# Performance work log

Hardware: AMD Instinct MI355X
Metric: run time of the kernel (lower is better)

The kernel has to match this reference:

```python
import jax, jax.numpy as jnp
import numpy as np

NH = 16      # n_head
HS = 64      # head_size
BD = 16      # bond_dim
HORIZON = 64
C = NH * HS  # n_embd = 1024


def setup_inputs() -> dict:
    key = jax.random.key(0)
    ks = jax.random.split(key, 16)
    B, T = 2, 1024
    s = lambda fan_in: 1.0 / np.sqrt(fan_in)
    inp = {
        'x': jax.random.normal(ks[0], (B, T, C), dtype=jnp.float32),
        # all linear weights stored (in, out) for x @ W
        'W_disp': jax.random.normal(ks[1], (C, NH * BD), dtype=jnp.float32) * s(C),
        'b_disp': jnp.zeros((NH * BD,), dtype=jnp.float32),
        'W_val': jax.random.normal(ks[2], (C, C), dtype=jnp.float32) * s(C),
        'b_val': jnp.zeros((C,), dtype=jnp.float32),
        'rel_pos_emb': jax.random.normal(ks[3], (HORIZON, BD), dtype=jnp.float32) * 0.02,
        'W_fused': jax.random.normal(ks[4], (BD, 2 * BD), dtype=jnp.float32) * s(BD),
        'b_fused': jnp.zeros((2 * BD,), dtype=jnp.float32),
        'W_pos': jax.random.normal(ks[5], (BD, BD), dtype=jnp.float32) * s(BD),
        'W_bond': jax.random.normal(ks[6], (BD, 1), dtype=jnp.float32) * s(BD),
        'b_bond': jnp.zeros((1,), dtype=jnp.float32),
        'W_dmg': jax.random.normal(ks[7], (BD, 1), dtype=jnp.float32) * s(BD),
        'b_dmg': jnp.full((1,), -3.0, dtype=jnp.float32),  # nn.init.constant_(-3.0)
        'W_cproj': jax.random.normal(ks[8], (C, C), dtype=jnp.float32) * s(C),
        'b_cproj': jnp.zeros((C,), dtype=jnp.float32),
    }
    return inp


def reference(x, W_disp, b_disp, W_val, b_val, rel_pos_emb, W_fused, b_fused,
              W_pos, W_bond, b_bond, W_dmg, b_dmg, W_cproj, b_cproj):
    B, T, Cm = x.shape
    delta = min(HORIZON, T)
    # projections -> (B, nh, T, d)
    disp = (x @ W_disp + b_disp).reshape(B, T, NH, BD).transpose(0, 2, 1, 3)
    val = (x @ W_val + b_val).reshape(B, T, NH, HS).transpose(0, 2, 1, 3)
    idx = jnp.arange(T)[:, None] + jnp.arange(delta)[None, :]  # (T, delta)
    disp_p = jnp.pad(disp, ((0, 0), (0, 0), (delta - 1, 0), (0, 0)))
    win = disp_p[:, :, idx]                       # (B, nh, T, delta, bd)
    strain = win - disp[:, :, :, None, :]         # (B, nh, T, delta, bd)
    pos_feat = rel_pos_emb @ W_pos                # (delta, bd)
    fused = strain @ W_fused + b_fused            # (B, nh, T, delta, 2*bd)
    bf, df = fused[..., :BD], fused[..., BD:]
    gelu = lambda z: jax.nn.gelu(z, approximate=False)
    bond_logits = (gelu(bf + pos_feat) @ W_bond + b_bond)[..., 0]   # (B,nh,T,delta)
    damage = jax.nn.sigmoid((gelu(df) @ W_dmg + b_dmg)[..., 0])
    bond_logits = bond_logits - damage * 10.0
    # causal validity mask: position t - delta + 1 + j must be >= 0
    cmask = (jnp.arange(T)[:, None] - delta + 1 + jnp.arange(delta)[None, :]) >= 0
    bond_logits = jnp.where(cmask[None, None], bond_logits, -jnp.inf)
    weights = jax.nn.softmax(bond_logits, axis=-1)
    val_p = jnp.pad(val, ((0, 0), (0, 0), (delta - 1, 0), (0, 0)))
    vwin = val_p[:, :, idx]                       # (B, nh, T, delta, hs)
    out = jnp.einsum('bhtd,bhtdk->bhtk', weights, vwin)  # (B, nh, T, hs)
    out = out.transpose(0, 2, 1, 3).reshape(B, T, Cm)
    return out @ W_cproj + b_cproj
```

## Files before the change

### kernel.cpp

```cpp
#include <hip/hip_runtime.h>
#include <math.h>


typedef __attribute__((ext_vector_type(4))) float f32x4;
typedef __attribute__((ext_vector_type(8))) __bf16 bf16x8;

__device__ __forceinline__ ushort f2bf(float f) {
    union { float f; unsigned u; } v; v.f = f;
    const unsigned r = v.u + 0x7fffu + ((v.u >> 16) & 1u);
    return (ushort)(r >> 16);
}

__device__ __forceinline__ float gelu_fast(float z) {
    const float a = -1.5957691216057308f * z * fmaf(0.044715f, z * z, 1.0f);
    return z * __builtin_amdgcn_rcpf(1.0f + __expf(a));
}

__global__ __launch_bounds__(256) void gemm_bf16_kernel(
    const ushort* __restrict__ A, const ushort* __restrict__ Bt,
    const float* __restrict__ bias, float* __restrict__ C,
    int M, int N, int K)
{
    __shared__ ushort As[64 * 64];
    __shared__ ushort Bs[64 * 64];
    const int tid  = threadIdx.x;
    const int wave = tid >> 6;
    const int lane = tid & 63;
    const int rowbase = blockIdx.y * 64;
    const int colbase = blockIdx.x * 64;
    const int wr = wave >> 1;
    const int wc = wave & 1;

    f32x4 acc[2][2] = {};

    for (int k0 = 0; k0 < K; k0 += 64) {
        #pragma unroll
        for (int i = 0; i < 2; ++i) {
            const int p   = i * 256 + tid;
            const int row = p >> 3;
            const int kc  = (p & 7) ^ (row & 7);
            const ushort* srcA = A + (size_t)(rowbase + row) * K + k0 + kc * 8;
            __builtin_amdgcn_global_load_lds(
                (const __attribute__((address_space(1))) void*)srcA,
                (__attribute__((address_space(3))) void*)(As + (size_t)p * 8),
                16, 0, 0);
            const ushort* srcB = Bt + (size_t)(colbase + row) * K + k0 + kc * 8;
            __builtin_amdgcn_global_load_lds(
                (const __attribute__((address_space(1))) void*)srcB,
                (__attribute__((address_space(3))) void*)(Bs + (size_t)p * 8),
                16, 0, 0);
        }
        __syncthreads();

        #pragma unroll
        for (int kk = 0; kk < 2; ++kk) {
            const int kb = kk * 32 + (lane >> 4) * 8;
            bf16x8 a[2], b[2];
            #pragma unroll
            for (int ni = 0; ni < 2; ++ni) {
                const int n = wc * 32 + ni * 16 + (lane & 15);
                const int off = (n * 128 + kb * 2) ^ ((n & 7) << 4);
                b[ni] = *(const bf16x8*)((const char*)Bs + off);
            }
            #pragma unroll
            for (int mi = 0; mi < 2; ++mi) {
                const int r = wr * 32 + mi * 16 + (lane & 15);
                const int off = (r * 128 + kb * 2) ^ ((r & 7) << 4);
                a[mi] = *(const bf16x8*)((const char*)As + off);
            }
            #pragma unroll
            for (int mi = 0; mi < 2; ++mi)
                #pragma unroll
                for (int ni = 0; ni < 2; ++ni)
                    acc[mi][ni] = __builtin_amdgcn_mfma_f32_16x16x32_bf16(
                        a[mi], b[ni], acc[mi][ni], 0, 0, 0);
        }
        __syncthreads();
    }

    #pragma unroll
    for (int mi = 0; mi < 2; ++mi)
        #pragma unroll
        for (int ni = 0; ni < 2; ++ni) {
            const int col = colbase + wc * 32 + ni * 16 + (lane & 15);
            const float bvc = bias[col];
            #pragma unroll
            for (int r = 0; r < 4; ++r) {
                const int row = rowbase + wr * 32 + mi * 16 + (lane >> 4) * 4 + r;
                C[(size_t)row * N + col] = acc[mi][ni][r] + bvc;
            }
        }
}

__global__ __launch_bounds__(256) void gemm_qv_kernel(
    const ushort* __restrict__ Acat,
    const ushort* __restrict__ xb,
    const float* __restrict__ b_val,
    float* __restrict__ dprojT,
    ushort* __restrict__ valT)
{
    __shared__ ushort As[128 * 64];
    __shared__ ushort Bs[64 * 64];
    const int tid  = threadIdx.x;
    const int wave = tid >> 6;
    const int lane = tid & 63;
    const int rowbase = blockIdx.y * 128;
    const int colbase = blockIdx.x * 64;
    const int wr = wave >> 1;
    const int wc = wave & 1;

    f32x4 acc[4][2] = {};

    for (int k0 = 0; k0 < 1024; k0 += 64) {
        #pragma unroll
        for (int i = 0; i < 4; ++i) {
            const int p   = i * 256 + tid;
            const int row = p >> 3;
            const int kc  = (p & 7) ^ (row & 7);
            const ushort* srcA = Acat + (size_t)(rowbase + row) * 1024 + k0 + kc * 8;
            __builtin_amdgcn_global_load_lds(
                (const __attribute__((address_space(1))) void*)srcA,
                (__attribute__((address_space(3))) void*)(As + (size_t)p * 8),
                16, 0, 0);
        }
        #pragma unroll
        for (int i = 0; i < 2; ++i) {
            const int p   = i * 256 + tid;
            const int row = p >> 3;
            const int kc  = (p & 7) ^ (row & 7);
            const ushort* srcB = xb + (size_t)(colbase + row) * 1024 + k0 + kc * 8;
            __builtin_amdgcn_global_load_lds(
                (const __attribute__((address_space(1))) void*)srcB,
                (__attribute__((address_space(3))) void*)(Bs + (size_t)p * 8),
                16, 0, 0);
        }
        __syncthreads();

        #pragma unroll
        for (int kk = 0; kk < 2; ++kk) {
            const int kb = kk * 32 + (lane >> 4) * 8;
            bf16x8 a[4], b[2];
            #pragma unroll
            for (int ni = 0; ni < 2; ++ni) {
                const int n = wc * 32 + ni * 16 + (lane & 15);
                const int off = (n * 128 + kb * 2) ^ ((n & 7) << 4);
                b[ni] = *(const bf16x8*)((const char*)Bs + off);
            }
            #pragma unroll
            for (int mi = 0; mi < 4; ++mi) {
                const int r = wr * 64 + mi * 16 + (lane & 15);
                const int off = (r * 128 + kb * 2) ^ ((r & 7) << 4);
                a[mi] = *(const bf16x8*)((const char*)As + off);
            }
            #pragma unroll
            for (int mi = 0; mi < 4; ++mi)
                #pragma unroll
                for (int ni = 0; ni < 2; ++ni)
                    acc[mi][ni] = __builtin_amdgcn_mfma_f32_16x16x32_bf16(
                        a[mi], b[ni], acc[mi][ni], 0, 0, 0);
        }
        __syncthreads();
    }

    if (rowbase < 512) {
        #pragma unroll
        for (int mi = 0; mi < 4; ++mi)
            #pragma unroll
            for (int ni = 0; ni < 2; ++ni) {
                const int col = colbase + wc * 32 + ni * 16 + (lane & 15);
                #pragma unroll
                for (int r = 0; r < 4; ++r) {
                    const int row = rowbase + wr * 64 + mi * 16 + (lane >> 4) * 4 + r;
                    dprojT[(size_t)row * 2048 + col] = acc[mi][ni][r];
                }
            }
    } else {
        #pragma unroll
        for (int mi = 0; mi < 4; ++mi)
            #pragma unroll
            for (int ni = 0; ni < 2; ++ni) {
                const int col = colbase + wc * 32 + ni * 16 + (lane & 15);
                #pragma unroll
                for (int r = 0; r < 4; ++r) {
                    const int row = rowbase - 512 + wr * 64 + mi * 16 + (lane >> 4) * 4 + r;
                    valT[(size_t)row * 2048 + col] = f2bf(acc[mi][ni][r] + b_val[row]);
                }
            }
    }
}

__global__ __launch_bounds__(256) void prep_kernel(
    const float* __restrict__ x,
    const float* __restrict__ W_disp,
    const float* __restrict__ W_val,
    const float* __restrict__ W_cproj,
    const float* __restrict__ W_fused,
    const float* __restrict__ rel,
    const float* __restrict__ Wpos,
    ushort* __restrict__ xb,
    ushort* __restrict__ Acat,
    ushort* __restrict__ WcT,
    float* __restrict__ posf)
{
    __shared__ float shmem[64 * 65];
    const int bid = blockIdx.x, tid = threadIdx.x;

    if (bid < 2048) {
        const int idx = bid * 256 + tid;
        const float4 v = reinterpret_cast<const float4*>(x)[idx];
        ushort4 o; o.x = f2bf(v.x); o.y = f2bf(v.y); o.z = f2bf(v.z); o.w = f2bf(v.w);
        reinterpret_cast<ushort4*>(xb)[idx] = o;
    } else if (bid < 2560) {
        const int isC = bid >= 2304;
        const int b2 = bid - (isC ? 2304 : 2048);
        const float* W = isC ? W_cproj : W_val;
        ushort* Wt = isC ? WcT : (Acat + 512 * 1024);
        const int n0 = (b2 & 15) * 64;
        const int k0 = (b2 >> 4) * 64;
        float (*tile)[65] = (float (*)[65])shmem;
        #pragma unroll
        for (int i = 0; i < 4; ++i) {
            const int idx = tid + i * 256;
            const int r = idx >> 4;
            const int c = (idx & 15) << 2;
            const float4 v = *reinterpret_cast<const float4*>(
                W + (size_t)(k0 + r) * 1024 + n0 + c);
            tile[r][c] = v.x; tile[r][c+1] = v.y; tile[r][c+2] = v.z; tile[r][c+3] = v.w;
        }
        __syncthreads();
        #pragma unroll
        for (int i = 0; i < 4; ++i) {
            const int idx = tid + i * 256;
            const int n = idx >> 4;
            const int c = (idx & 15) << 2;
            ushort4 o;
            o.x = f2bf(tile[c][n]);     o.y = f2bf(tile[c + 1][n]);
            o.z = f2bf(tile[c + 2][n]); o.w = f2bf(tile[c + 3][n]);
            *reinterpret_cast<ushort4*>(Wt + (size_t)(n0 + n) * 1024 + k0 + c) = o;
        }
    } else if (bid < 4608) {
        float* wfs = shmem;
        for (int i = tid; i < 512; i += 256) wfs[i] = W_fused[i];
        __syncthreads();
        const int idx = (bid - 2560) * 256 + tid;
        const int cc = idx >> 10;
        const int r  = idx & 1023;
        const int h = cc >> 5, e = cc & 31;
        const float* wd = W_disp + r * 256 + h * 16;
        float s = 0.f;
        #pragma unroll
        for (int d = 0; d < 16; ++d) s += wd[d] * wfs[d * 32 + e];
        Acat[idx] = f2bf(s);
    } else {
        for (int n = tid; n < 1024; n += 256) {
            const int j = n >> 4, e = n & 15;
            float s = 0.f;
            #pragma unroll
            for (int k = 0; k < 16; ++k) s += rel[j * 16 + k] * Wpos[k * 16 + e];
            posf[n] = s;
        }
    }
}

__global__ __launch_bounds__(256) void weights_kernel(
    const float* __restrict__ dprojT,
    const float* __restrict__ posf_g,
    const float* __restrict__ bfused,
    const float* __restrict__ Wbond,
    const float* __restrict__ bbond,
    const float* __restrict__ Wdmg,
    const float* __restrict__ bdmg,
    ushort* __restrict__ wout)
{
    __shared__ float dwin[32][68];
    __shared__ float sbd[16];
    __shared__ float wbd[16];
    __shared__ float wdm[16];
    const int tid  = threadIdx.x;
    const int wave = tid >> 6;
    const int lane = tid & 63;
    const int bh = blockIdx.x >> 8;
    const int t0 = (blockIdx.x & 255) * 4;
    const int h  = bh & 15;
    const int b  = bh >> 4;

    if (tid < 16) {
        sbd[tid] = bfused[16 + tid];
        wbd[tid] = Wbond[tid];
        wdm[tid] = Wdmg[tid];
    }
    const float* dbase = dprojT + (size_t)(h * 32) * 2048 + b * 1024;
    {
        const int r = tid & 63;
        int grow = t0 - 63 + r;
        grow = grow < 0 ? 0 : grow;
        #pragma unroll
        for (int i = 0; i < 8; ++i) {
            const int c = (tid >> 6) + i * 4;
            dwin[c][r] = dbase[(size_t)c * 2048 + grow];
        }
    }
    if (tid < 128) {
        const int c = tid >> 2;
        const int rs = tid & 3;
        if (rs < 3) {
            const int r = 64 + rs;
            int grow = t0 - 63 + r;
            dwin[c][r] = dbase[(size_t)c * 2048 + grow];
        }
    }
    float sbp[16];
    {
        const float4 p0 = *reinterpret_cast<const float4*>(posf_g + lane * 16);
        const float4 p1 = *reinterpret_cast<const float4*>(posf_g + lane * 16 + 4);
        const float4 p2 = *reinterpret_cast<const float4*>(posf_g + lane * 16 + 8);
        const float4 p3 = *reinterpret_cast<const float4*>(posf_g + lane * 16 + 12);
        sbp[0] = p0.x; sbp[1] = p0.y; sbp[2]  = p0.z; sbp[3]  = p0.w;
        sbp[4] = p1.x; sbp[5] = p1.y; sbp[6]  = p1.z; sbp[7]  = p1.w;
        sbp[8] = p2.x; sbp[9] = p2.y; sbp[10] = p2.z; sbp[11] = p2.w;
        sbp[12] = p3.x; sbp[13] = p3.y; sbp[14] = p3.z; sbp[15] = p3.w;
        #pragma unroll
        for (int e = 0; e < 16; ++e) sbp[e] += bfused[e];
    }
    __syncthreads();

    const int t = t0 + wave;
    const int tsrc = t + lane - 63;
    const int rw = wave + lane;
    const int rt = wave + 63;

    float bond = bbond[0];
    float dmg  = bdmg[0];
    #pragma unroll
    for (int e = 0; e < 16; ++e) {
        bond += gelu_fast(dwin[e][rw] - dwin[e][rt] + sbp[e]) * wbd[e];
        dmg  += gelu_fast(dwin[16 + e][rw] - dwin[16 + e][rt] + sbd[e]) * wdm[e];
    }
    const float damage = __builtin_amdgcn_rcpf(1.0f + __expf(-dmg));
    float logit = bond - 10.0f * damage;
    if (tsrc < 0) logit = -INFINITY;

    float m = logit;
    #pragma unroll
    for (int o = 32; o; o >>= 1) m = fmaxf(m, __shfl_xor(m, o));
    const float p = __expf(logit - m);
    float ssum = p;
    #pragma unroll
    for (int o = 32; o; o >>= 1) ssum += __shfl_xor(ssum, o);
    wout[(size_t)(bh * 1024 + t) * 64 + lane] = f2bf(p * __builtin_amdgcn_rcpf(ssum));
}

__global__ __launch_bounds__(256) void pv_kernel(
    const ushort* __restrict__ valT,
    const ushort* __restrict__ w,
    ushort* __restrict__ attnb)
{
    __shared__ ushort Ps[64 * 128];
    __shared__ ushort Vs[64 * 128];
    const int tid  = threadIdx.x;
    const int wave = tid >> 6;
    const int lane = tid & 63;
    const int bh = blockIdx.x >> 4;
    const int t0 = (blockIdx.x & 15) * 64;
    const int b  = bh >> 4;
    const int h  = bh & 15;

    #pragma unroll
    for (int i = 0; i < 4; ++i) {
        const int p = i * 256 + tid;
        const int c = p >> 4, q = p & 15;
        const int kc = q ^ (c & 7);
        int tt = t0 - 64 + kc * 8;
        tt = tt < 0 ? 0 : tt;
        const ushort* src = valT + (size_t)(h * 64 + c) * 2048 + b * 1024 + tt;
        __builtin_amdgcn_global_load_lds(
            (const __attribute__((address_space(1))) void*)src,
            (__attribute__((address_space(3))) void*)(Vs + (size_t)p * 8),
            16, 0, 0);
    }
    #pragma unroll
    for (int i = 0; i < 4; ++i)
        reinterpret_cast<uint4*>(Ps)[i * 256 + tid] = uint4{0, 0, 0, 0};
    __syncthreads();
    #pragma unroll
    for (int i = 0; i < 16; ++i) {
        const int n  = i * 256 + tid;
        const int ti = n >> 6, jj = n & 63;
        const ushort wv = w[((size_t)bh * 1024 + t0 + ti) * 64 + jj];
        const int off = (ti * 256 + (ti + jj + 1) * 2) ^ ((ti & 7) << 4);
        *(ushort*)((char*)Ps + off) = wv;
    }
    __syncthreads();

    const int wr = wave >> 1;
    const int wc = wave & 1;
    f32x4 acc[2][2] = {};
    #pragma unroll
    for (int kk = 0; kk < 4; ++kk) {
        const int kb = kk * 32 + (lane >> 4) * 8;
        bf16x8 a[2], bv[2];
        #pragma unroll
        for (int ni = 0; ni < 2; ++ni) {
            const int cc = wc * 32 + ni * 16 + (lane & 15);
            const int off = (cc * 256 + kb * 2) ^ ((cc & 7) << 4);
            bv[ni] = *(const bf16x8*)((const char*)Vs + off);
        }
        #pragma unroll
        for (int mi = 0; mi < 2; ++mi) {
            const int rr = wr * 32 + mi * 16 + (lane & 15);
            const int off = (rr * 256 + kb * 2) ^ ((rr & 7) << 4);
            a[mi] = *(const bf16x8*)((const char*)Ps + off);
        }
        #pragma unroll
        for (int mi = 0; mi < 2; ++mi)
            #pragma unroll
            for (int ni = 0; ni < 2; ++ni)
                acc[mi][ni] = __builtin_amdgcn_mfma_f32_16x16x32_bf16(
                    a[mi], bv[ni], acc[mi][ni], 0, 0, 0);
    }

    #pragma unroll
    for (int mi = 0; mi < 2; ++mi)
        #pragma unroll
        for (int ni = 0; ni < 2; ++ni) {
            const int c = wc * 32 + ni * 16 + (lane & 15);
            #pragma unroll
            for (int r = 0; r < 4; ++r) {
                const int trow = t0 + wr * 32 + mi * 16 + (lane >> 4) * 4 + r;
                attnb[(size_t)(b * 1024 + trow) * 1024 + h * 64 + c] =
                    f2bf(acc[mi][ni][r]);
            }
        }
}

extern "C" void kernel_launch(void* const* d_in, const int* in_sizes, int n_in,
                              void* d_out, int out_size, void* d_ws, size_t ws_size,
                              hipStream_t stream) {
    const float* x       = (const float*)d_in[0];
    const float* W_disp  = (const float*)d_in[1];
    const float* W_val   = (const float*)d_in[3];
    const float* b_val   = (const float*)d_in[4];
    const float* rel     = (const float*)d_in[5];
    const float* W_fused = (const float*)d_in[6];
    const float* b_fused = (const float*)d_in[7];
    const float* W_pos   = (const float*)d_in[8];
    const float* W_bond  = (const float*)d_in[9];
    const float* b_bond  = (const float*)d_in[10];
    const float* W_dmg   = (const float*)d_in[11];
    const float* b_dmg   = (const float*)d_in[12];
    const float* W_cproj = (const float*)d_in[13];
    const float* b_cproj = (const float*)d_in[14];
    float* out = (float*)d_out;

    ushort* Acat   = (ushort*)d_ws;
    ushort* xb     = Acat + 1536 * 1024;
    ushort* WcT    = xb + 2048 * 1024;
    float*  dprojT = (float*)(WcT + 1024 * 1024);
    ushort* valT   = (ushort*)(dprojT + 512 * 2048);
    ushort* wbuf   = valT + 1024 * 2048;
    ushort* attnb  = wbuf + 32768 * 64;
    float*  posf   = (float*)(attnb + 2048 * 1024);

    dim3 blk(256);
    prep_kernel<<<dim3(4609), blk, 0, stream>>>(
        x, W_disp, W_val, W_cproj, W_fused, rel, W_pos, xb, Acat, WcT, posf);
    gemm_qv_kernel<<<dim3(2048 / 64, 1536 / 128), blk, 0, stream>>>(
        Acat, xb, b_val, dprojT, valT);
    weights_kernel<<<dim3(8192), blk, 0, stream>>>(
        dprojT, posf, b_fused, W_bond, b_bond, W_dmg, b_dmg, wbuf);
    pv_kernel<<<dim3(512), blk, 0, stream>>>(valT, wbuf, attnb);
    gemm_bf16_kernel<<<dim3(1024 / 64, 2048 / 64), blk, 0, stream>>>(
        attnb, WcT, b_cproj, out, 2048, 1024, 1024);
}
```

Before: 76.89 us.

## Fuse bond-weight softmax into PV kernel, swizzle GEMM blocks, enlarge cproj tile

Merges weights_kernel and pv_kernel so each PV block computes its 64x64 softmax bond weights directly into shared memory. This drops the global round trip of the bf16 weight buffer and one launch. It also adds an XCD-aware block-index swizzle to the QV GEMM and replaces the generic cproj GEMM with a 128x64-tile version that uses the same swizzle. The trade-off is fewer, heavier blocks in the fused kernel (512 blocks, more LDS), which lowers parallelism for the GELU-heavy weight computation.

```diff
diff --git a/kernel.cpp b/kernel.cpp
--- a/kernel.cpp
+++ b/kernel.cpp
@@ -14,82 +14,6 @@
 __device__ __forceinline__ float gelu_fast(float z) {
     const float a = -1.5957691216057308f * z * fmaf(0.044715f, z * z, 1.0f);
     return z * __builtin_amdgcn_rcpf(1.0f + __expf(a));
-}
-
-__global__ __launch_bounds__(256) void gemm_bf16_kernel(
-    const ushort* __restrict__ A, const ushort* __restrict__ Bt,
-    const float* __restrict__ bias, float* __restrict__ C,
-    int M, int N, int K)
-{
-    __shared__ ushort As[64 * 64];
-    __shared__ ushort Bs[64 * 64];
-    const int tid  = threadIdx.x;
-    const int wave = tid >> 6;
-    const int lane = tid & 63;
-    const int rowbase = blockIdx.y * 64;
-    const int colbase = blockIdx.x * 64;
-    const int wr = wave >> 1;
-    const int wc = wave & 1;
-
-    f32x4 acc[2][2] = {};
-
-    for (int k0 = 0; k0 < K; k0 += 64) {
-        #pragma unroll
-        for (int i = 0; i < 2; ++i) {
-            const int p   = i * 256 + tid;
-            const int row = p >> 3;
-            const int kc  = (p & 7) ^ (row & 7);
-            const ushort* srcA = A + (size_t)(rowbase + row) * K + k0 + kc * 8;
-            __builtin_amdgcn_global_load_lds(
-                (const __attribute__((address_space(1))) void*)srcA,
-                (__attribute__((address_space(3))) void*)(As + (size_t)p * 8),
-                16, 0, 0);
-            const ushort* srcB = Bt + (size_t)(colbase + row) * K + k0 + kc * 8;
-            __builtin_amdgcn_global_load_lds(
-                (const __attribute__((address_space(1))) void*)srcB,
-                (__attribute__((address_space(3))) void*)(Bs + (size_t)p * 8),
-                16, 0, 0);
-        }
-        __syncthreads();
-
-        #pragma unroll
-        for (int kk = 0; kk < 2; ++kk) {
-            const int kb = kk * 32 + (lane >> 4) * 8;
-            bf16x8 a[2], b[2];
-            #pragma unroll
-            for (int ni = 0; ni < 2; ++ni) {
-                const int n = wc * 32 + ni * 16 + (lane & 15);
-                const int off = (n * 128 + kb * 2) ^ ((n & 7) << 4);
-                b[ni] = *(const bf16x8*)((const char*)Bs + off);
-            }
-            #pragma unroll
-            for (int mi = 0; mi < 2; ++mi) {
-                const int r = wr * 32 + mi * 16 + (lane & 15);
-                const int off = (r * 128 + kb * 2) ^ ((r & 7) << 4);
-                a[mi] = *(const bf16x8*)((const char*)As + off);
-            }
-            #pragma unroll
-            for (int mi = 0; mi < 2; ++mi)
-                #pragma unroll
-                for (int ni = 0; ni < 2; ++ni)
-                    acc[mi][ni] = __builtin_amdgcn_mfma_f32_16x16x32_bf16(
-                        a[mi], b[ni], acc[mi][ni], 0, 0, 0);
-        }
-        __syncthreads();
-    }
-
-    #pragma unroll
-    for (int mi = 0; mi < 2; ++mi)
-        #pragma unroll
-        for (int ni = 0; ni < 2; ++ni) {
-            const int col = colbase + wc * 32 + ni * 16 + (lane & 15);
-            const float bvc = bias[col];
-            #pragma unroll
-            for (int r = 0; r < 4; ++r) {
-                const int row = rowbase + wr * 32 + mi * 16 + (lane >> 4) * 4 + r;
-                C[(size_t)row * N + col] = acc[mi][ni][r] + bvc;
-            }
-        }
 }
 
 __global__ __launch_bounds__(256) void gemm_qv_kernel(
@@ -104,8 +28,10 @@
     const int tid  = threadIdx.x;
     const int wave = tid >> 6;
     const int lane = tid & 63;
-    const int rowbase = blockIdx.y * 128;
-    const int colbase = blockIdx.x * 64;
+    const int bid  = blockIdx.x;
+    const int swz  = (bid & 7) * 48 + (bid >> 3);
+    const int rowbase = (swz >> 5) * 128;
+    const int colbase = (swz & 31) * 64;
     const int wr = wave >> 1;
     const int wc = wave & 1;
 
@@ -187,6 +113,91 @@
                 }
             }
     }
+}
+
+__global__ __launch_bounds__(256) void gemm_cproj_kernel(
+    const ushort* __restrict__ A,
+    const ushort* __restrict__ Bt,
+    const float* __restrict__ bias,
+    float* __restrict__ C)
+{
+    __shared__ ushort As[128 * 64];
+    __shared__ ushort Bs[64 * 64];
+    const int tid  = threadIdx.x;
+    const int wave = tid >> 6;
+    const int lane = tid & 63;
+    const int bid  = blockIdx.x;
+    const int swz  = (bid & 7) * 32 + (bid >> 3);
+    const int rowbase = (swz >> 4) * 128;
+    const int colbase = (swz & 15) * 64;
+    const int wr = wave >> 1;
+    const int wc = wave & 1;
+
+    f32x4 acc[4][2] = {};
+
+    for (int k0 = 0; k0 < 1024; k0 += 64) {
+        #pragma unroll
+        for (int i = 0; i < 4; ++i) {
+            const int p   = i * 256 + tid;
+            const int row = p >> 3;
+            const int kc  = (p & 7) ^ (row & 7);
+            const ushort* srcA = A + (size_t)(rowbase + row) * 1024 + k0 + kc * 8;
+            __builtin_amdgcn_global_load_lds(
+                (const __attribute__((address_space(1))) void*)srcA,
+                (__attribute__((address_space(3))) void*)(As + (size_t)p * 8),
+                16, 0, 0);
+        }
+        #pragma unroll
+        for (int i = 0; i < 2; ++i) {
+            const int p   = i * 256 + tid;
+            const int row = p >> 3;
+            const int kc  = (p & 7) ^ (row & 7);
+            const ushort* srcB = Bt + (size_t)(colbase + row) * 1024 + k0 + kc * 8;
+            __builtin_amdgcn_global_load_lds(
+                (const __attribute__((address_space(1))) void*)srcB,
+                (__attribute__((address_space(3))) void*)(Bs + (size_t)p * 8),
+                16, 0, 0);
+        }
+        __syncthreads();
+
+        #pragma unroll
+        for (int kk = 0; kk < 2; ++kk) {
+            const int kb = kk * 32 + (lane >> 4) * 8;
+            bf16x8 a[4], b[2];
+            #pragma unroll
+            for (int ni = 0; ni < 2; ++ni) {
+                const int n = wc * 32 + ni * 16 + (lane & 15);
+                const int off = (n * 128 + kb * 2) ^ ((n & 7) << 4);
+                b[ni] = *(const bf16x8*)((const char*)Bs + off);
+            }
+            #pragma unroll
+            for (int mi = 0; mi < 4; ++mi) {
+                const int r = wr * 64 + mi * 16 + (lane & 15);
+                const int off = (r * 128 + kb * 2) ^ ((r & 7) << 4);
+                a[mi] = *(const bf16x8*)((const char*)As + off);
+            }
+            #pragma unroll
+            for (int mi = 0; mi < 4; ++mi)
+                #pragma unroll
+                for (int ni = 0; ni < 2; ++ni)
+                    acc[mi][ni] = __builtin_amdgcn_mfma_f32_16x16x32_bf16(
+                        a[mi], b[ni], acc[mi][ni], 0, 0, 0);
+        }
+        __syncthreads();
+    }
+
+    #pragma unroll
+    for (int mi = 0; mi < 4; ++mi)
+        #pragma unroll
+        for (int ni = 0; ni < 2; ++ni) {
+            const int col = colbase + wc * 32 + ni * 16 + (lane & 15);
+            const float bvc = bias[col];
+            #pragma unroll
+            for (int r = 0; r < 4; ++r) {
+                const int row = rowbase + wr * 64 + mi * 16 + (lane >> 4) * 4 + r;
+                C[(size_t)row * 1024 + col] = acc[mi][ni][r] + bvc;
+            }
+        }
 }
 
 __global__ __launch_bounds__(256) void prep_kernel(
@@ -262,106 +273,29 @@
     }
 }
 
-__global__ __launch_bounds__(256) void weights_kernel(
+__global__ __launch_bounds__(256) void wpv_kernel(
     const float* __restrict__ dprojT,
+    const ushort* __restrict__ valT,
     const float* __restrict__ posf_g,
     const float* __restrict__ bfused,
     const float* __restrict__ Wbond,
     const float* __restrict__ bbond,
     const float* __restrict__ Wdmg,
     const float* __restrict__ bdmg,
-    ushort* __restrict__ wout)
+    ushort* __restrict__ attnb)
 {
-    __shared__ float dwin[32][68];
-    __shared__ float sbd[16];
-    __shared__ float wbd[16];
-    __shared__ float wdm[16];
+    __shared__ float2 dwin[16][128];
+    __shared__ ushort Ps[64 * 128];
+    __shared__ ushort Vs[64 * 128];
+    __shared__ float sbd_s[16], wbd_s[16], wdm_s[16];
+
     const int tid  = threadIdx.x;
     const int wave = tid >> 6;
     const int lane = tid & 63;
-    const int bh = blockIdx.x >> 8;
-    const int t0 = (blockIdx.x & 255) * 4;
-    const int h  = bh & 15;
-    const int b  = bh >> 4;
-
-    if (tid < 16) {
-        sbd[tid] = bfused[16 + tid];
-        wbd[tid] = Wbond[tid];
-        wdm[tid] = Wdmg[tid];
-    }
-    const float* dbase = dprojT + (size_t)(h * 32) * 2048 + b * 1024;
-    {
-        const int r = tid & 63;
-        int grow = t0 - 63 + r;
-        grow = grow < 0 ? 0 : grow;
-        #pragma unroll
-        for (int i = 0; i < 8; ++i) {
-            const int c = (tid >> 6) + i * 4;
-            dwin[c][r] = dbase[(size_t)c * 2048 + grow];
-        }
-    }
-    if (tid < 128) {
-        const int c = tid >> 2;
-        const int rs = tid & 3;
-        if (rs < 3) {
-            const int r = 64 + rs;
-            int grow = t0 - 63 + r;
-            dwin[c][r] = dbase[(size_t)c * 2048 + grow];
-        }
-    }
-    float sbp[16];
-    {
-        const float4 p0 = *reinterpret_cast<const float4*>(posf_g + lane * 16);
-        const float4 p1 = *reinterpret_cast<const float4*>(posf_g + lane * 16 + 4);
-        const float4 p2 = *reinterpret_cast<const float4*>(posf_g + lane * 16 + 8);
-        const float4 p3 = *reinterpret_cast<const float4*>(posf_g + lane * 16 + 12);
-        sbp[0] = p0.x; sbp[1] = p0.y; sbp[2]  = p0.z; sbp[3]  = p0.w;
-        sbp[4] = p1.x; sbp[5] = p1.y; sbp[6]  = p1.z; sbp[7]  = p1.w;
-        sbp[8] = p2.x; sbp[9] = p2.y; sbp[10] = p2.z; sbp[11] = p2.w;
-        sbp[12] = p3.x; sbp[13] = p3.y; sbp[14] = p3.z; sbp[15] = p3.w;
-        #pragma unroll
-        for (int e = 0; e < 16; ++e) sbp[e] += bfused[e];
-    }
-    __syncthreads();
-
-    const int t = t0 + wave;
-    const int tsrc = t + lane - 63;
-    const int rw = wave + lane;
-    const int rt = wave + 63;
-
-    float bond = bbond[0];
-    float dmg  = bdmg[0];
-    #pragma unroll
-    for (int e = 0; e < 16; ++e) {
-        bond += gelu_fast(dwin[e][rw] - dwin[e][rt] + sbp[e]) * wbd[e];
-        dmg  += gelu_fast(dwin[16 + e][rw] - dwin[16 + e][rt] + sbd[e]) * wdm[e];
-    }
-    const float damage = __builtin_amdgcn_rcpf(1.0f + __expf(-dmg));
-    float logit = bond - 10.0f * damage;
-    if (tsrc < 0) logit = -INFINITY;
-
-    float m = logit;
-    #pragma unroll
-    for (int o = 32; o; o >>= 1) m = fmaxf(m, __shfl_xor(m, o));
-    const float p = __expf(logit - m);
-    float ssum = p;
-    #pragma unroll
-    for (int o = 32; o; o >>= 1) ssum += __shfl_xor(ssum, o);
-    wout[(size_t)(bh * 1024 + t) * 64 + lane] = f2bf(p * __builtin_amdgcn_rcpf(ssum));
-}
-
-__global__ __launch_bounds__(256) void pv_kernel(
-    const ushort* __restrict__ valT,
-    const ushort* __restrict__ w,
-    ushort* __restrict__ attnb)
-{
-    __shared__ ushort Ps[64 * 128];
-    __shared__ ushort Vs[64 * 128];
-    const int tid  = threadIdx.x;
-    const int wave = tid >> 6;
-    const int lane = tid & 63;
-    const int bh = blockIdx.x >> 4;
-    const int t0 = (blockIdx.x & 15) * 64;
+    const int bid  = blockIdx.x;
+    const int swz  = (bid & 7) * 64 + (bid >> 3);
+    const int bh = swz >> 4;
+    const int t0 = (swz & 15) * 64;
     const int b  = bh >> 4;
     const int h  = bh & 15;
 
@@ -378,16 +312,72 @@
             (__attribute__((address_space(3))) void*)(Vs + (size_t)p * 8),
             16, 0, 0);
     }
+    if (tid < 16) {
+        sbd_s[tid] = bfused[16 + tid];
+        wbd_s[tid] = Wbond[tid];
+        wdm_s[tid] = Wdmg[tid];
+    }
     #pragma unroll
     for (int i = 0; i < 4; ++i)
         reinterpret_cast<uint4*>(Ps)[i * 256 + tid] = uint4{0, 0, 0, 0};
+    const float* dbase = dprojT + (size_t)(h * 32) * 2048 + b * 1024;
+    for (int n = tid; n < 4096; n += 256) {
+        const int c = n >> 7, r = n & 127;
+        int grow = t0 - 63 + r;
+        grow = grow < 0 ? 0 : (grow > 1023 ? 1023 : grow);
+        ((float*)dwin)[(c >> 1) * 256 + r * 2 + (c & 1)] =
+            dbase[(size_t)c * 2048 + grow];
+    }
+    float sbp[16];
+    {
+        const float4 p0 = *reinterpret_cast<const float4*>(posf_g + lane * 16);
+        const float4 p1 = *reinterpret_cast<const float4*>(posf_g + lane * 16 + 4);
+        const float4 p2 = *reinterpret_cast<const float4*>(posf_g + lane * 16 + 8);
+        const float4 p3 = *reinterpret_cast<const float4*>(posf_g + lane * 16 + 12);
+        sbp[0] = p0.x; sbp[1] = p0.y; sbp[2]  = p0.z; sbp[3]  = p0.w;
+        sbp[4] = p1.x; sbp[5] = p1.y; sbp[6]  = p1.z; sbp[7]  = p1.w;
+        sbp[8] = p2.x; sbp[9] = p2.y; sbp[10] = p2.z; sbp[11] = p2.w;
+        sbp[12] = p3.x; sbp[13] = p3.y; sbp[14] = p3.z; sbp[15] = p3.w;
+        #pragma unroll
+        for (int e = 0; e < 16; ++e) sbp[e] += bfused[e];
+    }
+    const float bb = bbond[0];
+    const float bd = bdmg[0];
     __syncthreads();
-    #pragma unroll
+
     for (int i = 0; i < 16; ++i) {
-        const int n  = i * 256 + tid;
-        const int ti = n >> 6, jj = n & 63;
-        const ushort wv = w[((size_t)bh * 1024 + t0 + ti) * 64 + jj];
-        const int off = (ti * 256 + (ti + jj + 1) * 2) ^ ((ti & 7) << 4);
+        const int toff = (wave << 4) + i;
+        const int rw = toff + lane;
+        const int rt = toff + 63;
+        float bond = bb, dmg = bd;
+        #pragma unroll
+        for (int e2 = 0; e2 < 8; ++e2) {
+            const float2 aw = dwin[e2][rw];
+            const float2 at = dwin[e2][rt];
+            bond += gelu_fast(aw.x - at.x + sbp[e2 * 2 + 0]) * wbd_s[e2 * 2 + 0];
+            bond += gelu_fast(aw.y - at.y + sbp[e2 * 2 + 1]) * wbd_s[e2 * 2 + 1];
+        }
+        #pragma unroll
+        for (int e2 = 8; e2 < 16; ++e2) {
+            const float2 aw = dwin[e2][rw];
+            const float2 at = dwin[e2][rt];
+            const int e = (e2 - 8) * 2;
+            dmg += gelu_fast(aw.x - at.x + sbd_s[e + 0]) * wdm_s[e + 0];
+            dmg += gelu_fast(aw.y - at.y + sbd_s[e + 1]) * wdm_s[e + 1];
+        }
+        const float damage = __builtin_amdgcn_rcpf(1.0f + __expf(-dmg));
+        float logit = bond - 10.0f * damage;
+        if (t0 + toff + lane - 63 < 0) logit = -INFINITY;
+
+        float m = logit;
+        #pragma unroll
+        for (int o = 32; o; o >>= 1) m = fmaxf(m, __shfl_xor(m, o));
+        const float p = __expf(logit - m);
+        float ssum = p;
+        #pragma unroll
+        for (int o = 32; o; o >>= 1) ssum += __shfl_xor(ssum, o);
+        const ushort wv = f2bf(p * __builtin_amdgcn_rcpf(ssum));
+        const int off = (toff * 256 + (toff + lane + 1) * 2) ^ ((toff & 7) << 4);
         *(ushort*)((char*)Ps + off) = wv;
     }
     __syncthreads();
@@ -457,18 +447,16 @@
     ushort* WcT    = xb + 2048 * 1024;
     float*  dprojT = (float*)(WcT + 1024 * 1024);
     ushort* valT   = (ushort*)(dprojT + 512 * 2048);
-    ushort* wbuf   = valT + 1024 * 2048;
-    ushort* attnb  = wbuf + 32768 * 64;
+    ushort* attnb  = valT + 1024 * 2048;
     float*  posf   = (float*)(attnb + 2048 * 1024);
 
     dim3 blk(256);
     prep_kernel<<<dim3(4609), blk, 0, stream>>>(
         x, W_disp, W_val, W_cproj, W_fused, rel, W_pos, xb, Acat, WcT, posf);
-    gemm_qv_kernel<<<dim3(2048 / 64, 1536 / 128), blk, 0, stream>>>(
+    gemm_qv_kernel<<<dim3(384), blk, 0, stream>>>(
         Acat, xb, b_val, dprojT, valT);
-    weights_kernel<<<dim3(8192), blk, 0, stream>>>(
-        dprojT, posf, b_fused, W_bond, b_bond, W_dmg, b_dmg, wbuf);
-    pv_kernel<<<dim3(512), blk, 0, stream>>>(valT, wbuf, attnb);
-    gemm_bf16_kernel<<<dim3(1024 / 64, 2048 / 64), blk, 0, stream>>>(
-        attnb, WcT, b_cproj, out, 2048, 1024, 1024);
-}
+    wpv_kernel<<<dim3(512), blk, 0, stream>>>(
+        dprojT, valT, posf, b_fused, W_bond, b_bond, W_dmg, b_dmg, attnb);
+    gemm_cproj_kernel<<<dim3(256), blk, 0, stream>>>(
+        attnb, WcT, b_cproj, out);
+}
```

After: 82.68 us. 7.5% more time.

## Double-buffer LDS in both GEMMs and process 16 timesteps per weights block

Applied to the files above, without the earlier changes.

Both bf16 GEMM kernels now use two LDS buffers, so the async global-to-LDS load of the next K tile is issued before the MFMA work on the current tile. This hides load latency behind compute. The weights kernel now has each block handle 16 timesteps (4 per wave) instead of 4. That cuts the grid to a quarter and loads each sliding window of displacement data once per 16 outputs, reducing redundant global reads. The cost is doubled LDS per GEMM block, which may lower occupancy, and fewer blocks for the weights kernel.

```diff
diff --git a/kernel.cpp b/kernel.cpp
--- a/kernel.cpp
+++ b/kernel.cpp
@@ -16,13 +16,121 @@
     return z * __builtin_amdgcn_rcpf(1.0f + __expf(a));
 }
 
-__global__ __launch_bounds__(256) void gemm_bf16_kernel(
-    const ushort* __restrict__ A, const ushort* __restrict__ Bt,
-    const float* __restrict__ bias, float* __restrict__ C,
-    int M, int N, int K)
+__global__ __launch_bounds__(256) void gemm_qv_kernel(
+    const ushort* __restrict__ Acat,
+    const ushort* __restrict__ xb,
+    const float* __restrict__ b_val,
+    float* __restrict__ dprojT,
+    ushort* __restrict__ valT)
 {
-    __shared__ ushort As[64 * 64];
-    __shared__ ushort Bs[64 * 64];
+    __shared__ ushort As[2][128 * 64];
+    __shared__ ushort Bs[2][64 * 64];
+    const int tid  = threadIdx.x;
+    const int wave = tid >> 6;
+    const int lane = tid & 63;
+    const int rowbase = blockIdx.y * 128;
+    const int colbase = blockIdx.x * 64;
+    const int wr = wave >> 1;
+    const int wc = wave & 1;
+
+    f32x4 acc[4][2] = {};
+
+    auto stage = [&](int buf, int k0) {
+        #pragma unroll
+        for (int i = 0; i < 4; ++i) {
+            const int p   = i * 256 + tid;
+            const int row = p >> 3;
+            const int kc  = (p & 7) ^ (row & 7);
+            const ushort* srcA = Acat + (size_t)(rowbase + row) * 1024 + k0 + kc * 8;
+            __builtin_amdgcn_global_load_lds(
+                (const __attribute__((address_space(1))) void*)srcA,
+                (__attribute__((address_space(3))) void*)(&As[buf][p * 8]),
+                16, 0, 0);
+        }
+        #pragma unroll
+        for (int i = 0; i < 2; ++i) {
+            const int p   = i * 256 + tid;
+            const int row = p >> 3;
+            const int kc  = (p & 7) ^ (row & 7);
+            const ushort* srcB = xb + (size_t)(colbase + row) * 1024 + k0 + kc * 8;
+            __builtin_amdgcn_global_load_lds(
+                (const __attribute__((address_space(1))) void*)srcB,
+                (__attribute__((address_space(3))) void*)(&Bs[buf][p * 8]),
+                16, 0, 0);
+        }
+    };
+    auto compute = [&](int buf) {
+        #pragma unroll
+        for (int kk = 0; kk < 2; ++kk) {
+            const int kb = kk * 32 + (lane >> 4) * 8;
+            bf16x8 a[4], b[2];
+            #pragma unroll
+            for (int ni = 0; ni < 2; ++ni) {
+                const int n = wc * 32 + ni * 16 + (lane & 15);
+                const int off = (n * 128 + kb * 2) ^ ((n & 7) << 4);
+                b[ni] = *(const bf16x8*)((const char*)Bs[buf] + off);
+            }
+            #pragma unroll
+            for (int mi = 0; mi < 4; ++mi) {
+                const int r = wr * 64 + mi * 16 + (lane & 15);
+                const int off = (r * 128 + kb * 2) ^ ((r & 7) << 4);
+                a[mi] = *(const bf16x8*)((const char*)As[buf] + off);
+            }
+            #pragma unroll
+            for (int mi = 0; mi < 4; ++mi)
+                #pragma unroll
+                for (int ni = 0; ni < 2; ++ni)
+                    acc[mi][ni] = __builtin_amdgcn_mfma_f32_16x16x32_bf16(
+                        a[mi], b[ni], acc[mi][ni], 0, 0, 0);
+        }
+    };
+
+    stage(0, 0);
+    __syncthreads();
+    for (int kt = 0; kt < 16; kt += 2) {
+        if (kt + 1 < 16) stage(1, (kt + 1) * 64);
+        compute(0);
+        __syncthreads();
+        if (kt + 2 < 16) stage(0, (kt + 2) * 64);
+        compute(1);
+        __syncthreads();
+    }
+
+    if (rowbase < 512) {
+        #pragma unroll
+        for (int mi = 0; mi < 4; ++mi)
+            #pragma unroll
+            for (int ni = 0; ni < 2; ++ni) {
+                const int col = colbase + wc * 32 + ni * 16 + (lane & 15);
+                #pragma unroll
+                for (int r = 0; r < 4; ++r) {
+                    const int row = rowbase + wr * 64 + mi * 16 + (lane >> 4) * 4 + r;
+                    dprojT[(size_t)row * 2048 + col] = acc[mi][ni][r];
+                }
+            }
+    } else {
+        #pragma unroll
+        for (int mi = 0; mi < 4; ++mi)
+            #pragma unroll
+            for (int ni = 0; ni < 2; ++ni) {
+                const int col = colbase + wc * 32 + ni * 16 + (lane & 15);
+                #pragma unroll
+                for (int r = 0; r < 4; ++r) {
+                    const int row = rowbase - 512 + wr * 64 + mi * 16 + (lane >> 4) * 4 + r;
+                    valT[(size_t)row * 2048 + col] = f2bf(acc[mi][ni][r] + b_val[row]);
+                }
+            }
+    }
+}
+
+__global__ __launch_bounds__(256) void gemm_cproj_kernel(
+    const ushort* __restrict__ A,
+    const ushort* __restrict__ Bt,
+    const float* __restrict__ bias,
+    float* __restrict__ C)
+{
+    __shared__ ushort As[2][64 * 64];
+    __shared__ ushort Bs[2][64 * 64];
     const int tid  = threadIdx.x;
     const int wave = tid >> 6;
     const int lane = tid & 63;
@@ -33,25 +141,25 @@
 
     f32x4 acc[2][2] = {};
 
-    for (int k0 = 0; k0 < K; k0 += 64) {
+    auto stage = [&](int buf, int k0) {
         #pragma unroll
         for (int i = 0; i < 2; ++i) {
             const int p   = i * 256 + tid;
             const int row = p >> 3;
             const int kc  = (p & 7) ^ (row & 7);
-            const ushort* srcA = A + (size_t)(rowbase + row) * K + k0 + kc * 8;
+            const ushort* srcA = A + (size_t)(rowbase + row) * 1024 + k0 + kc * 8;
             __builtin_amdgcn_global_load_lds(
                 (const __attribute__((address_space(1))) void*)srcA,
-                (__attribute__((address_space(3))) void*)(As + (size_t)p * 8),
+                (__attribute__((address_space(3))) void*)(&As[buf][p * 8]),
                 16, 0, 0);
-            const ushort* srcB = Bt + (size_t)(colbase + row) * K + k0 + kc * 8;
+            const ushort* srcB = Bt + (size_t)(colbase + row) * 1024 + k0 + kc * 8;
             __builtin_amdgcn_global_load_lds(
                 (const __attribute__((address_space(1))) void*)srcB,
-                (__attribute__((address_space(3))) void*)(Bs + (size_t)p * 8),
+                (__attribute__((address_space(3))) void*)(&Bs[buf][p * 8]),
                 16, 0, 0);
         }
-        __syncthreads();
-
+    };
+    auto compute = [&](int buf) {
         #pragma unroll
         for (int kk = 0; kk < 2; ++kk) {
             const int kb = kk * 32 + (lane >> 4) * 8;
@@ -60,13 +168,13 @@
             for (int ni = 0; ni < 2; ++ni) {
                 const int n = wc * 32 + ni * 16 + (lane & 15);
                 const int off = (n * 128 + kb * 2) ^ ((n & 7) << 4);
-                b[ni] = *(const bf16x8*)((const char*)Bs + off);
+                b[ni] = *(const bf16x8*)((const char*)Bs[buf] + off);
             }
             #pragma unroll
             for (int mi = 0; mi < 2; ++mi) {
                 const int r = wr * 32 + mi * 16 + (lane & 15);
                 const int off = (r * 128 + kb * 2) ^ ((r & 7) << 4);
-                a[mi] = *(const bf16x8*)((const char*)As + off);
+                a[mi] = *(const bf16x8*)((const char*)As[buf] + off);
             }
             #pragma unroll
             for (int mi = 0; mi < 2; ++mi)
@@ -75,6 +183,16 @@
                     acc[mi][ni] = __builtin_amdgcn_mfma_f32_16x16x32_bf16(
                         a[mi], b[ni], acc[mi][ni], 0, 0, 0);
         }
+    };
+
+    stage(0, 0);
+    __syncthreads();
+    for (int kt = 0; kt < 16; kt += 2) {
+        if (kt + 1 < 16) stage(1, (kt + 1) * 64);
+        compute(0);
+        __syncthreads();
+        if (kt + 2 < 16) stage(0, (kt + 2) * 64);
+        compute(1);
         __syncthreads();
     }
 
@@ -87,106 +205,9 @@
             #pragma unroll
             for (int r = 0; r < 4; ++r) {
                 const int row = rowbase + wr * 32 + mi * 16 + (lane >> 4) * 4 + r;
-                C[(size_t)row * N + col] = acc[mi][ni][r] + bvc;
-            }
-        }
-}
-
-__global__ __launch_bounds__(256) void gemm_qv_kernel(
-    const ushort* __restrict__ Acat,
-    const ushort* __restrict__ xb,
-    const float* __restrict__ b_val,
-    float* __restrict__ dprojT,
-    ushort* __restrict__ valT)
-{
-    __shared__ ushort As[128 * 64];
-    __shared__ ushort Bs[64 * 64];
-    const int tid  = threadIdx.x;
-    const int wave = tid >> 6;
-    const int lane = tid & 63;
-    const int rowbase = blockIdx.y * 128;
-    const int colbase = blockIdx.x * 64;
-    const int wr = wave >> 1;
-    const int wc = wave & 1;
-
-    f32x4 acc[4][2] = {};
-
-    for (int k0 = 0; k0 < 1024; k0 += 64) {
-        #pragma unroll
-        for (int i = 0; i < 4; ++i) {
-            const int p   = i * 256 + tid;
-            const int row = p >> 3;
-            const int kc  = (p & 7) ^ (row & 7);
-            const ushort* srcA = Acat + (size_t)(rowbase + row) * 1024 + k0 + kc * 8;
-            __builtin_amdgcn_global_load_lds(
-                (const __attribute__((address_space(1))) void*)srcA,
-                (__attribute__((address_space(3))) void*)(As + (size_t)p * 8),
-                16, 0, 0);
-        }
-        #pragma unroll
-        for (int i = 0; i < 2; ++i) {
-            const int p   = i * 256 + tid;
-            const int row = p >> 3;
-            const int kc  = (p & 7) ^ (row & 7);
-            const ushort* srcB = xb + (size_t)(colbase + row) * 1024 + k0 + kc * 8;
-            __builtin_amdgcn_global_load_lds(
-                (const __attribute__((address_space(1))) void*)srcB,
-                (__attribute__((address_space(3))) void*)(Bs + (size_t)p * 8),
-                16, 0, 0);
-        }
-        __syncthreads();
-
-        #pragma unroll
-        for (int kk = 0; kk < 2; ++kk) {
-            const int kb = kk * 32 + (lane >> 4) * 8;
-            bf16x8 a[4], b[2];
-            #pragma unroll
-            for (int ni = 0; ni < 2; ++ni) {
-                const int n = wc * 32 + ni * 16 + (lane & 15);
-                const int off = (n * 128 + kb * 2) ^ ((n & 7) << 4);
-                b[ni] = *(const bf16x8*)((const char*)Bs + off);
-            }
-            #pragma unroll
-            for (int mi = 0; mi < 4; ++mi) {
-                const int r = wr * 64 + mi * 16 + (lane & 15);
-                const int off = (r * 128 + kb * 2) ^ ((r & 7) << 4);
-                a[mi] = *(const bf16x8*)((const char*)As + off);
-            }
-            #pragma unroll
-            for (int mi = 0; mi < 4; ++mi)
-                #pragma unroll
-                for (int ni = 0; ni < 2; ++ni)
-                    acc[mi][ni] = __builtin_amdgcn_mfma_f32_16x16x32_bf16(
-                        a[mi], b[ni], acc[mi][ni], 0, 0, 0);
-        }
-        __syncthreads();
-    }
-
-    if (rowbase < 512) {
-        #pragma unroll
-        for (int mi = 0; mi < 4; ++mi)
-            #pragma unroll
-            for (int ni = 0; ni < 2; ++ni) {
-                const int col = colbase + wc * 32 + ni * 16 + (lane & 15);
-                #pragma unroll
-                for (int r = 0; r < 4; ++r) {
-                    const int row = rowbase + wr * 64 + mi * 16 + (lane >> 4) * 4 + r;
-                    dprojT[(size_t)row * 2048 + col] = acc[mi][ni][r];
-                }
-            }
-    } else {
-        #pragma unroll
-        for (int mi = 0; mi < 4; ++mi)
-            #pragma unroll
-            for (int ni = 0; ni < 2; ++ni) {
-                const int col = colbase + wc * 32 + ni * 16 + (lane & 15);
-                #pragma unroll
-                for (int r = 0; r < 4; ++r) {
-                    const int row = rowbase - 512 + wr * 64 + mi * 16 + (lane >> 4) * 4 + r;
-                    valT[(size_t)row * 2048 + col] = f2bf(acc[mi][ni][r] + b_val[row]);
-                }
-            }
-    }
+                C[(size_t)row * 1024 + col] = acc[mi][ni][r] + bvc;
+            }
+        }
 }
 
 __global__ __launch_bounds__(256) void prep_kernel(
@@ -272,42 +293,28 @@
     const float* __restrict__ bdmg,
     ushort* __restrict__ wout)
 {
-    __shared__ float dwin[32][68];
-    __shared__ float sbd[16];
-    __shared__ float wbd[16];
-    __shared__ float wdm[16];
+    __shared__ float dwin[32][80];
+    __shared__ float sbd_s[16], wbd_s[16], wdm_s[16];
     const int tid  = threadIdx.x;
     const int wave = tid >> 6;
     const int lane = tid & 63;
-    const int bh = blockIdx.x >> 8;
-    const int t0 = (blockIdx.x & 255) * 4;
+    const int bh = blockIdx.x >> 6;
+    const int t0 = (blockIdx.x & 63) * 16;
     const int h  = bh & 15;
     const int b  = bh >> 4;
 
     if (tid < 16) {
-        sbd[tid] = bfused[16 + tid];
-        wbd[tid] = Wbond[tid];
-        wdm[tid] = Wdmg[tid];
+        sbd_s[tid] = bfused[16 + tid];
+        wbd_s[tid] = Wbond[tid];
+        wdm_s[tid] = Wdmg[tid];
     }
     const float* dbase = dprojT + (size_t)(h * 32) * 2048 + b * 1024;
-    {
-        const int r = tid & 63;
+    for (int n = tid; n < 2560; n += 256) {
+        const int c = n / 80;
+        const int r = n % 80;
         int grow = t0 - 63 + r;
-        grow = grow < 0 ? 0 : grow;
-        #pragma unroll
-        for (int i = 0; i < 8; ++i) {
-            const int c = (tid >> 6) + i * 4;
-            dwin[c][r] = dbase[(size_t)c * 2048 + grow];
-        }
-    }
-    if (tid < 128) {
-        const int c = tid >> 2;
-        const int rs = tid & 3;
-        if (rs < 3) {
-            const int r = 64 + rs;
-            int grow = t0 - 63 + r;
-            dwin[c][r] = dbase[(size_t)c * 2048 + grow];
-        }
+        grow = grow < 0 ? 0 : (grow > 1023 ? 1023 : grow);
+        dwin[c][r] = dbase[(size_t)c * 2048 + grow];
     }
     float sbp[16];
     {
@@ -322,32 +329,35 @@
         #pragma unroll
         for (int e = 0; e < 16; ++e) sbp[e] += bfused[e];
     }
+    const float bb = bbond[0];
+    const float bd = bdmg[0];
     __syncthreads();
 
-    const int t = t0 + wave;
-    const int tsrc = t + lane - 63;
-    const int rw = wave + lane;
-    const int rt = wave + 63;
-
-    float bond = bbond[0];
-    float dmg  = bdmg[0];
-    #pragma unroll
-    for (int e = 0; e < 16; ++e) {
-        bond += gelu_fast(dwin[e][rw] - dwin[e][rt] + sbp[e]) * wbd[e];
-        dmg  += gelu_fast(dwin[16 + e][rw] - dwin[16 + e][rt] + sbd[e]) * wdm[e];
-    }
-    const float damage = __builtin_amdgcn_rcpf(1.0f + __expf(-dmg));
-    float logit = bond - 10.0f * damage;
-    if (tsrc < 0) logit = -INFINITY;
-
-    float m = logit;
-    #pragma unroll
-    for (int o = 32; o; o >>= 1) m = fmaxf(m, __shfl_xor(m, o));
-    const float p = __expf(logit - m);
-    float ssum = p;
-    #pragma unroll
-    for (int o = 32; o; o >>= 1) ssum += __shfl_xor(ssum, o);
-    wout[(size_t)(bh * 1024 + t) * 64 + lane] = f2bf(p * __builtin_amdgcn_rcpf(ssum));
+    #pragma unroll
+    for (int i = 0; i < 4; ++i) {
+        const int k = wave * 4 + i;
+        const int t = t0 + k;
+        const int rw = k + lane;
+        const int rt = k + 63;
+        float bond = bb, dmg = bd;
+        #pragma unroll
+        for (int e = 0; e < 16; ++e) {
+            bond += gelu_fast(dwin[e][rw] - dwin[e][rt] + sbp[e]) * wbd_s[e];
+            dmg  += gelu_fast(dwin[16 + e][rw] - dwin[16 + e][rt] + sbd_s[e]) * wdm_s[e];
+        }
+        const float damage = __builtin_amdgcn_rcpf(1.0f + __expf(-dmg));
+        float logit = bond - 10.0f * damage;
+        if (t + lane - 63 < 0) logit = -INFINITY;
+
+        float m = logit;
+        #pragma unroll
+        for (int o = 32; o; o >>= 1) m = fmaxf(m, __shfl_xor(m, o));
+        const float p = __expf(logit - m);
+        float ssum = p;
+        #pragma unroll
+        for (int o = 32; o; o >>= 1) ssum += __shfl_xor(ssum, o);
+        wout[(size_t)(bh * 1024 + t) * 64 + lane] = f2bf(p * __builtin_amdgcn_rcpf(ssum));
+    }
 }
 
 __global__ __launch_bounds__(256) void pv_kernel(
@@ -466,9 +476,9 @@
         x, W_disp, W_val, W_cproj, W_fused, rel, W_pos, xb, Acat, WcT, posf);
     gemm_qv_kernel<<<dim3(2048 / 64, 1536 / 128), blk, 0, stream>>>(
         Acat, xb, b_val, dprojT, valT);
-    weights_kernel<<<dim3(8192), blk, 0, stream>>>(
+    weights_kernel<<<dim3(2048), blk, 0, stream>>>(
         dprojT, posf, b_fused, W_bond, b_bond, W_dmg, b_dmg, wbuf);
     pv_kernel<<<dim3(512), blk, 0, stream>>>(valT, wbuf, attnb);
-    gemm_bf16_kernel<<<dim3(1024 / 64, 2048 / 64), blk, 0, stream>>>(
-        attnb, WcT, b_cproj, out, 2048, 1024, 1024);
-}
+    gemm_cproj_kernel<<<dim3(1024 / 64, 2048 / 64), blk, 0, stream>>>(
+        attnb, WcT, b_cproj, out);
+}
```

Measured after the change: 85.32 us. 11.0% more time.
